# Performance work log

Hardware: AMD Instinct MI355X
Metric: run time of the kernel (lower is better)

The kernel has to match this reference:

```python
import jax, jax.numpy as jnp
import numpy as np

B, LQ, LK = 8, 1024, 1024
H, HD = 8, 128            # n_head, hidden_dim (per-head)
HEAD_DIM, CHILD_DIM = 512, 512
D_MODEL = HEAD_DIM + CHILD_DIM
TEMP = float(np.sqrt(HD))
NEG = 100000000.0
EPS = 1e-5


def setup_inputs() -> dict:
    key = jax.random.key(0)
    ks = jax.random.split(key, 12)
    q = jax.random.normal(ks[0], (B, LQ, HEAD_DIM), jnp.float32)
    k = jax.random.normal(ks[1], (B, LK, CHILD_DIM), jnp.float32)
    v = jax.random.normal(ks[2], (B, LK, D_MODEL), jnp.float32)
    old_score = 0.1 * jax.random.normal(ks[3], (H * B, LQ, LK), jnp.float32)
    float_mask = (jax.random.uniform(ks[4], (B, LQ, LK)) > 0.2).astype(jnp.float32)
    # torch nn.Linear weights are [out_features, in_features]
    wq = jax.random.normal(ks[5], (H * HD, HEAD_DIM), jnp.float32) * np.sqrt(2.0 / (HEAD_DIM + HD))
    wk = jax.random.normal(ks[6], (H * HD, CHILD_DIM), jnp.float32) * np.sqrt(2.0 / (CHILD_DIM + HD))
    wv = jax.random.normal(ks[7], (H * HD, D_MODEL), jnp.float32) * np.sqrt(2.0 / (D_MODEL + HD))
    wfc = jax.random.normal(ks[8], (D_MODEL, H * HD), jnp.float32) * np.sqrt(2.0 / (D_MODEL + H * HD))
    bq = jnp.zeros((H * HD,), jnp.float32)
    bk = jnp.zeros((H * HD,), jnp.float32)
    bv = jnp.zeros((H * HD,), jnp.float32)
    bfc = jnp.zeros((D_MODEL,), jnp.float32)
    ln_g = jnp.ones((D_MODEL,), jnp.float32)
    ln_b = jnp.zeros((D_MODEL,), jnp.float32)
    return dict(q=q, k=k, v=v, old_score=old_score, float_mask=float_mask,
                wq=wq, bq=bq, wk=wk, bk=bk, wv=wv, bv=bv,
                wfc=wfc, bfc=bfc, ln_g=ln_g, ln_b=ln_b)


def reference(q, k, v, old_score, float_mask, wq, bq, wk, bk, wv, bv, wfc, bfc, ln_g, ln_b):
    b, lq, _ = q.shape
    lk = k.shape[1]
    residual = v
    qh = (q @ wq.T + bq).reshape(b, lq, H, HD)   # [b,lq,h,d]
    kh = (k @ wk.T + bk).reshape(b, lk, H, HD)
    vh = (v @ wv.T + bv).reshape(b, lk, H, HD)
    # raw_score laid out head-major to match torch's (n_head*B, Lq, Lk)
    raw = jnp.einsum('bqhd,bkhd->hbqk', qh, kh) + old_score.reshape(H, b, lq, lk)
    score = raw - NEG * (1.0 - float_mask)[None]          # broadcast over heads
    attn = jax.nn.softmax(score / TEMP, axis=-1)          # eval path
    out = jnp.einsum('hbqk,bkhd->bqhd', attn, vh).reshape(b, lq, H * HD)
    out = out @ wfc.T + bfc + residual                    # dropout=identity (eval)
    mean = jnp.mean(out, axis=-1, keepdims=True)
    var = jnp.mean(jnp.square(out - mean), axis=-1, keepdims=True)
    out = (out - mean) / jnp.sqrt(var + EPS) * ln_g + ln_b
    return out, raw.reshape(H * b, lq, lk)
```

## Files before the change

kernel.cpp:

```cpp
#include <hip/hip_runtime.h>

typedef unsigned short u16;
typedef __bf16 bf16x8 __attribute__((ext_vector_type(8)));
typedef float f32x4 __attribute__((ext_vector_type(4)));

#define MFMA16(a,b,c) __builtin_amdgcn_mfma_f32_16x16x32_bf16(a,b,c,0,0,0)

static __device__ __forceinline__ u16 f2bf(float f){
  unsigned u = __builtin_bit_cast(unsigned, f);
  u += 0x7fffu + ((u>>16)&1u);
  return (u16)(u>>16);
}
static __device__ __forceinline__ int swz256(int r,int c){ return r*256 + (c ^ ((r&7)<<4)); }
static __device__ __forceinline__ int swz128(int r,int c){ return r*128 + (c ^ ((r&7)<<4)); }

__global__ void conv_f2b(const float* __restrict__ in, u16* __restrict__ out, int n4){
  int i = blockIdx.x*256 + threadIdx.x;
  if (i >= n4) return;
  float4 f = reinterpret_cast<const float4*>(in)[i];
  ushort4 o; o.x=f2bf(f.x); o.y=f2bf(f.y); o.z=f2bf(f.z); o.w=f2bf(f.w);
  reinterpret_cast<ushort4*>(out)[i] = o;
}

template<int MODE>
__global__ __launch_bounds__(256) void gemm_nt(const u16* __restrict__ A, const u16* __restrict__ Bw,
    const float* __restrict__ bias, const float* __restrict__ resid,
    u16* __restrict__ Cb, float* __restrict__ Cf, int M, int N, int K)
{
  __shared__ uint4 ldsv[2048];
  char* la = (char*)ldsv;
  char* lb = la + 16384;
  const int tid = threadIdx.x, lane = tid&63, w = tid>>6;
  const int l15 = lane&15, l4 = lane>>4;
  const int wm = w&1, wn = w>>1;
  const int mb = blockIdx.x, nb = blockIdx.y;
  const f32x4 zero4 = {0.f,0.f,0.f,0.f};
  f32x4 acc[4][4];
  #pragma unroll
  for (int i=0;i<4;++i)
    #pragma unroll
    for (int j=0;j<4;++j) acc[i][j] = zero4;

  for (int k0=0;k0<K;k0+=64){
    __syncthreads();
    #pragma unroll
    for (int it=0; it<4; ++it){
      int idx = tid + it*256;
      int row = idx>>3, c = idx&7;
      uint4 va = *reinterpret_cast<const uint4*>(A + (size_t)(mb*128+row)*K + k0 + c*8);
      *reinterpret_cast<uint4*>(la + swz128(row, c*16)) = va;
      uint4 vb = *reinterpret_cast<const uint4*>(Bw + (size_t)(nb*128+row)*K + k0 + c*8);
      *reinterpret_cast<uint4*>(lb + swz128(row, c*16)) = vb;
    }
    __syncthreads();
    #pragma unroll
    for (int kk=0;kk<2;++kk){
      bf16x8 af[4], bfr[4];
      #pragma unroll
      for (int i=0;i<4;++i){
        af[i]  = *reinterpret_cast<const bf16x8*>(la + swz128(wm*64+i*16+l15, (kk*32+l4*8)*2));
        bfr[i] = *reinterpret_cast<const bf16x8*>(lb + swz128(wn*64+i*16+l15, (kk*32+l4*8)*2));
      }
      #pragma unroll
      for (int i=0;i<4;++i)
        #pragma unroll
        for (int j=0;j<4;++j)
          acc[i][j] = MFMA16(af[i], bfr[j], acc[i][j]);
    }
  }
  #pragma unroll
  for (int j=0;j<4;++j){
    int col = nb*128 + wn*64 + j*16 + l15;
    float bv = bias[col];
    #pragma unroll
    for (int i=0;i<4;++i){
      int row0 = mb*128 + wm*64 + i*16 + l4*4;
      if (MODE == 0){
        #pragma unroll
        for (int r=0;r<4;++r)
          Cb[(size_t)(row0+r)*N + col] = f2bf(acc[i][j][r] + bv);
      } else if (MODE == 1){
        int bb = row0 >> 10, kp = row0 & 1023;
        ushort4 o;
        o.x = f2bf(acc[i][j][0]+bv); o.y = f2bf(acc[i][j][1]+bv);
        o.z = f2bf(acc[i][j][2]+bv); o.w = f2bf(acc[i][j][3]+bv);
        *reinterpret_cast<ushort4*>(Cb + (size_t)(bb*1024+col)*1024 + kp) = o;
      } else {
        #pragma unroll
        for (int r=0;r<4;++r){
          size_t off = (size_t)(row0+r)*N + col;
          Cf[off] = acc[i][j][r] + bv + resid[off];
        }
      }
    }
  }
}

__global__ __launch_bounds__(256) void attn_fused(const u16* __restrict__ qh,
    const u16* __restrict__ kh, const u16* __restrict__ vt,
    const float* __restrict__ oldsc, const float* __restrict__ fmask,
    float* __restrict__ raw, u16* __restrict__ ao)
{
  __shared__ uint4 ldsv[2560];
  char* lk_ = (char*)ldsv;
  char* lv_ = lk_ + 16384;
  char* lp_ = lk_ + 32768;
  const int tid = threadIdx.x, lane = tid&63, w = tid>>6;
  const int l15 = lane&15, l4 = lane>>4;
  const int qb = blockIdx.x, b = blockIdx.y, h = blockIdx.z;
  const float invT = 0.088388347648318447f;
  const f32x4 zero4 = {0.f,0.f,0.f,0.f};

  bf16x8 qf[4];
  {
    const u16* qp = qh + (size_t)(b*1024 + qb*64 + w*16 + l15)*1024 + h*128 + l4*8;
    #pragma unroll
    for (int kk=0;kk<4;++kk)
      qf[kk] = __builtin_bit_cast(bf16x8, *reinterpret_cast<const uint4*>(qp + kk*32));
  }
  f32x4 oacc[8];
  #pragma unroll
  for (int i=0;i<8;++i) oacc[i] = zero4;
  float mr[4], lr[4];
  #pragma unroll
  for (int r=0;r<4;++r){ mr[r] = -3.0e38f; lr[r] = 0.f; }

  for (int kt=0; kt<16; ++kt){
    __syncthreads();
    #pragma unroll
    for (int it=0; it<4; ++it){
      int idx = tid + it*256;
      { int row = idx>>4, c = idx&15;
        uint4 t = *reinterpret_cast<const uint4*>(kh + (size_t)(b*1024 + kt*64 + row)*1024 + h*128 + c*8);
        *reinterpret_cast<uint4*>(lk_ + swz256(row, c*16)) = t; }
      { int row = idx>>3, c = idx&7;
        uint4 t = *reinterpret_cast<const uint4*>(vt + (size_t)(b*1024 + h*128 + row)*1024 + kt*64 + c*8);
        *reinterpret_cast<uint4*>(lv_ + swz128(row, c*16)) = t; }
    }
    __syncthreads();
    f32x4 fs[4];
    #pragma unroll
    for (int fj=0;fj<4;++fj){
      f32x4 s = zero4;
      #pragma unroll
      for (int kk=0;kk<4;++kk){
        bf16x8 kf = *reinterpret_cast<const bf16x8*>(lk_ + swz256(fj*16+l15, (kk*32+l4*8)*2));
        s = MFMA16(qf[kk], kf, s);
      }
      fs[fj] = s;
    }
    const int qglob = qb*64 + w*16 + l4*4;
    size_t rbase  = ((size_t)(h*8 + b)*1024 + qglob)*1024 + kt*64;
    size_t mbase2 = ((size_t)b*1024 + qglob)*1024 + kt*64;
    float tm[4];
    #pragma unroll
    for (int r=0;r<4;++r){
      float mx = -3.0e38f;
      #pragma unroll
      for (int fj=0;fj<4;++fj){
        int kvc = fj*16 + l15;
        float old = oldsc[rbase + (size_t)r*1024 + kvc];
        float rv = fs[fj][r] + old;
        raw[rbase + (size_t)r*1024 + kvc] = rv;
        float mk = fmask[mbase2 + (size_t)r*1024 + kvc];
        float sc = (rv - 1.0e8f*(1.0f - mk)) * invT;
        fs[fj][r] = sc;
        mx = fmaxf(mx, sc);
      }
      tm[r] = mx;
    }
    #pragma unroll
    for (int o=1;o<16;o<<=1){
      #pragma unroll
      for (int r=0;r<4;++r) tm[r] = fmaxf(tm[r], __shfl_xor(tm[r], o));
    }
    #pragma unroll
    for (int r=0;r<4;++r){
      float mn  = fmaxf(mr[r], tm[r]);
      float esc = __expf(mr[r] - mn);
      mr[r] = mn;
      lr[r] *= esc;
      #pragma unroll
      for (int nf=0;nf<8;++nf) oacc[nf][r] *= esc;
      int prow = w*16 + l4*4 + r;
      #pragma unroll
      for (int fj=0;fj<4;++fj){
        float p = __expf(fs[fj][r] - mn);
        lr[r] += p;
        *reinterpret_cast<u16*>(lp_ + swz128(prow, (fj*16+l15)*2)) = f2bf(p);
      }
    }
    #pragma unroll
    for (int kkv=0;kkv<2;++kkv){
      bf16x8 pf = *reinterpret_cast<const bf16x8*>(lp_ + swz128(w*16+l15, (kkv*32+l4*8)*2));
      #pragma unroll
      for (int nf=0;nf<8;++nf){
        bf16x8 vf = *reinterpret_cast<const bf16x8*>(lv_ + swz128(nf*16+l15, (kkv*32+l4*8)*2));
        oacc[nf] = MFMA16(pf, vf, oacc[nf]);
      }
    }
  }
  #pragma unroll
  for (int o=1;o<16;o<<=1){
    #pragma unroll
    for (int r=0;r<4;++r) lr[r] += __shfl_xor(lr[r], o);
  }
  #pragma unroll
  for (int nf=0;nf<8;++nf){
    int col = h*128 + nf*16 + l15;
    #pragma unroll
    for (int r=0;r<4;++r){
      size_t orow = (size_t)(b*1024 + qb*64 + w*16 + l4*4 + r);
      ao[orow*1024 + col] = f2bf(oacc[nf][r] * (1.0f/lr[r]));
    }
  }
}

__global__ __launch_bounds__(256) void ln_k(float* __restrict__ io,
    const float* __restrict__ g, const float* __restrict__ bb)
{
  const int lane = threadIdx.x & 63, w = threadIdx.x >> 6;
  size_t row = (size_t)blockIdx.x*4 + w;
  float4* p = reinterpret_cast<float4*>(io + row*1024);
  float4 x[4];
  float s = 0.f, s2 = 0.f;
  #pragma unroll
  for (int i=0;i<4;++i){
    x[i] = p[lane + i*64];
    s  += x[i].x + x[i].y + x[i].z + x[i].w;
    s2 += x[i].x*x[i].x + x[i].y*x[i].y + x[i].z*x[i].z + x[i].w*x[i].w;
  }
  #pragma unroll
  for (int o=1;o<64;o<<=1){ s += __shfl_xor(s,o); s2 += __shfl_xor(s2,o); }
  float mean = s * 0.0009765625f;
  float var  = s2 * 0.0009765625f - mean*mean;
  float rstd = rsqrtf(var + 1e-5f);
  const float4* gp = reinterpret_cast<const float4*>(g);
  const float4* bp = reinterpret_cast<const float4*>(bb);
  #pragma unroll
  for (int i=0;i<4;++i){
    float4 gg = gp[lane+i*64], bv = bp[lane+i*64], y;
    y.x = (x[i].x-mean)*rstd*gg.x + bv.x;
    y.y = (x[i].y-mean)*rstd*gg.y + bv.y;
    y.z = (x[i].z-mean)*rstd*gg.z + bv.z;
    y.w = (x[i].w-mean)*rstd*gg.w + bv.w;
    p[lane+i*64] = y;
  }
}

extern "C" void kernel_launch(void* const* d_in, const int* in_sizes, int n_in,
                              void* d_out, int out_size, void* d_ws, size_t ws_size,
                              hipStream_t stream)
{
  const float* q    = (const float*)d_in[0];
  const float* k    = (const float*)d_in[1];
  const float* v    = (const float*)d_in[2];
  const float* olds = (const float*)d_in[3];
  const float* fm   = (const float*)d_in[4];
  const float* wq   = (const float*)d_in[5];
  const float* bq   = (const float*)d_in[6];
  const float* wk   = (const float*)d_in[7];
  const float* bk   = (const float*)d_in[8];
  const float* wv   = (const float*)d_in[9];
  const float* bv   = (const float*)d_in[10];
  const float* wfc  = (const float*)d_in[11];
  const float* bfc  = (const float*)d_in[12];
  const float* lng  = (const float*)d_in[13];
  const float* lnb  = (const float*)d_in[14];
  float* out = (float*)d_out;
  float* raw = out + 8388608;

  u16* ws  = (u16*)d_ws;
  u16* qbf = ws;
  u16* kbf = qbf + 4194304;
  u16* vbf = kbf + 4194304;
  u16* wqb = vbf + 8388608;
  u16* wkb = wqb + 524288;
  u16* wvb = wkb + 524288;
  u16* wfb = wvb + 1048576;
  u16* qhb = wfb + 1048576;
  u16* khb = qhb + 8388608;
  u16* vtb = khb + 8388608;
  u16* aob = vtb + 8388608;

  conv_f2b<<<4096,256,0,stream>>>(q,   qbf, 1048576);
  conv_f2b<<<4096,256,0,stream>>>(k,   kbf, 1048576);
  conv_f2b<<<8192,256,0,stream>>>(v,   vbf, 2097152);
  conv_f2b<<<512, 256,0,stream>>>(wq,  wqb, 131072);
  conv_f2b<<<512, 256,0,stream>>>(wk,  wkb, 131072);
  conv_f2b<<<1024,256,0,stream>>>(wv,  wvb, 262144);
  conv_f2b<<<1024,256,0,stream>>>(wfc, wfb, 262144);

  gemm_nt<0><<<dim3(64,8),256,0,stream>>>(qbf, wqb, bq, nullptr, qhb, nullptr, 8192,1024,512);
  gemm_nt<0><<<dim3(64,8),256,0,stream>>>(kbf, wkb, bk, nullptr, khb, nullptr, 8192,1024,512);
  gemm_nt<1><<<dim3(64,8),256,0,stream>>>(vbf, wvb, bv, nullptr, vtb, nullptr, 8192,1024,1024);

  attn_fused<<<dim3(16,8,8),256,0,stream>>>(qhb, khb, vtb, olds, fm, raw, aob);

  gemm_nt<2><<<dim3(64,8),256,0,stream>>>(aob, wfb, bfc, v, nullptr, out, 8192,1024,1024);
  ln_k<<<2048,256,0,stream>>>(out, lng, lnb);
}
```

Before: 319.2 us.

## Use direct global-to-LDS loads and vectorize score/mask/raw accesses in attention

Replaces register-staged global loads plus LDS stores with global_load_lds direct-to-LDS transfers in both the GEMM and attention kernels, pre-swizzling source columns so the MFMA read layout is preserved. In attention, K rows are permuted so each lane's four score columns are contiguous, which turns the old_score and mask reads and the raw store into float4 accesses and the P write into a single ushort4 store. The old_score and mask loads are also issued before the barrier so they overlap with the tile load. The approach depends on the row permutation and swizzle exactly matching what the MFMA fragment reads expect, so any mismatch would give wrong results.

```diff
diff --git a/kernel.cpp b/kernel.cpp
--- a/kernel.cpp
+++ b/kernel.cpp
@@ -13,6 +13,12 @@
 }
 static __device__ __forceinline__ int swz256(int r,int c){ return r*256 + (c ^ ((r&7)<<4)); }
 static __device__ __forceinline__ int swz128(int r,int c){ return r*128 + (c ^ ((r&7)<<4)); }
+
+static __device__ __forceinline__ void gload16(const void* g, void* l){
+  __builtin_amdgcn_global_load_lds(
+      (const __attribute__((address_space(1))) unsigned int*)g,
+      (__attribute__((address_space(3))) unsigned int*)l, 16, 0, 0);
+}
 
 __global__ void conv_f2b(const float* __restrict__ in, u16* __restrict__ out, int n4){
   int i = blockIdx.x*256 + threadIdx.x;
@@ -45,12 +51,10 @@
     __syncthreads();
     #pragma unroll
     for (int it=0; it<4; ++it){
-      int idx = tid + it*256;
-      int row = idx>>3, c = idx&7;
-      uint4 va = *reinterpret_cast<const uint4*>(A + (size_t)(mb*128+row)*K + k0 + c*8);
-      *reinterpret_cast<uint4*>(la + swz128(row, c*16)) = va;
-      uint4 vb = *reinterpret_cast<const uint4*>(Bw + (size_t)(nb*128+row)*K + k0 + c*8);
-      *reinterpret_cast<uint4*>(lb + swz128(row, c*16)) = vb;
+      int slot = it*256 + tid;
+      int r = slot>>3, cg = (slot&7) ^ (r&7);
+      gload16(A + (size_t)(mb*128+r)*K + k0 + cg*8, la + (it*256 + w*64)*16);
+      gload16(Bw + (size_t)(nb*128+r)*K + k0 + cg*8, lb + (it*256 + w*64)*16);
     }
     __syncthreads();
     #pragma unroll
@@ -125,17 +129,29 @@
   #pragma unroll
   for (int r=0;r<4;++r){ mr[r] = -3.0e38f; lr[r] = 0.f; }
 
+  const int qglob = qb*64 + w*16 + l4*4;
+
   for (int kt=0; kt<16; ++kt){
     __syncthreads();
     #pragma unroll
     for (int it=0; it<4; ++it){
-      int idx = tid + it*256;
-      { int row = idx>>4, c = idx&15;
-        uint4 t = *reinterpret_cast<const uint4*>(kh + (size_t)(b*1024 + kt*64 + row)*1024 + h*128 + c*8);
-        *reinterpret_cast<uint4*>(lk_ + swz256(row, c*16)) = t; }
-      { int row = idx>>3, c = idx&7;
-        uint4 t = *reinterpret_cast<const uint4*>(vt + (size_t)(b*1024 + h*128 + row)*1024 + kt*64 + c*8);
-        *reinterpret_cast<uint4*>(lv_ + swz128(row, c*16)) = t; }
+      int slot = it*256 + tid;
+      { int rs = slot>>4, cs = slot&15;
+        int cg = cs ^ (rs&7);
+        int kv = (rs&15)*4 + (rs>>4);
+        gload16(kh + (size_t)(b*1024 + kt*64 + kv)*1024 + h*128 + cg*8,
+                lk_ + (it*256 + w*64)*16); }
+      { int r = slot>>3, cg = (slot&7) ^ (r&7);
+        gload16(vt + (size_t)(b*1024 + h*128 + r)*1024 + kt*64 + cg*8,
+                lv_ + (it*256 + w*64)*16); }
+    }
+    size_t rbase = ((size_t)(h*8 + b)*1024 + qglob)*1024 + kt*64 + l15*4;
+    size_t mbase = ((size_t)b*1024 + qglob)*1024 + kt*64 + l15*4;
+    float4 o4[4], m4[4];
+    #pragma unroll
+    for (int r=0;r<4;++r){
+      o4[r] = *reinterpret_cast<const float4*>(oldsc + rbase + (size_t)r*1024);
+      m4[r] = *reinterpret_cast<const float4*>(fmask + mbase + (size_t)r*1024);
     }
     __syncthreads();
     f32x4 fs[4];
@@ -149,25 +165,18 @@
       }
       fs[fj] = s;
     }
-    const int qglob = qb*64 + w*16 + l4*4;
-    size_t rbase  = ((size_t)(h*8 + b)*1024 + qglob)*1024 + kt*64;
-    size_t mbase2 = ((size_t)b*1024 + qglob)*1024 + kt*64;
     float tm[4];
     #pragma unroll
     for (int r=0;r<4;++r){
-      float mx = -3.0e38f;
-      #pragma unroll
-      for (int fj=0;fj<4;++fj){
-        int kvc = fj*16 + l15;
-        float old = oldsc[rbase + (size_t)r*1024 + kvc];
-        float rv = fs[fj][r] + old;
-        raw[rbase + (size_t)r*1024 + kvc] = rv;
-        float mk = fmask[mbase2 + (size_t)r*1024 + kvc];
-        float sc = (rv - 1.0e8f*(1.0f - mk)) * invT;
-        fs[fj][r] = sc;
-        mx = fmaxf(mx, sc);
-      }
-      tm[r] = mx;
+      float4 rv;
+      rv.x = fs[0][r] + o4[r].x; rv.y = fs[1][r] + o4[r].y;
+      rv.z = fs[2][r] + o4[r].z; rv.w = fs[3][r] + o4[r].w;
+      *reinterpret_cast<float4*>(raw + rbase + (size_t)r*1024) = rv;
+      fs[0][r] = (rv.x - 1.0e8f*(1.0f - m4[r].x)) * invT;
+      fs[1][r] = (rv.y - 1.0e8f*(1.0f - m4[r].y)) * invT;
+      fs[2][r] = (rv.z - 1.0e8f*(1.0f - m4[r].z)) * invT;
+      fs[3][r] = (rv.w - 1.0e8f*(1.0f - m4[r].w)) * invT;
+      tm[r] = fmaxf(fmaxf(fs[0][r], fs[1][r]), fmaxf(fs[2][r], fs[3][r]));
     }
     #pragma unroll
     for (int o=1;o<16;o<<=1){
@@ -182,13 +191,13 @@
       lr[r] *= esc;
       #pragma unroll
       for (int nf=0;nf<8;++nf) oacc[nf][r] *= esc;
+      float px = __expf(fs[0][r] - mn), py = __expf(fs[1][r] - mn);
+      float pz = __expf(fs[2][r] - mn), pw = __expf(fs[3][r] - mn);
+      lr[r] += px + py + pz + pw;
+      ushort4 o;
+      o.x = f2bf(px); o.y = f2bf(py); o.z = f2bf(pz); o.w = f2bf(pw);
       int prow = w*16 + l4*4 + r;
-      #pragma unroll
-      for (int fj=0;fj<4;++fj){
-        float p = __expf(fs[fj][r] - mn);
-        lr[r] += p;
-        *reinterpret_cast<u16*>(lp_ + swz128(prow, (fj*16+l15)*2)) = f2bf(p);
-      }
+      *reinterpret_cast<ushort4*>(lp_ + swz128(prow, l15*8)) = o;
     }
     #pragma unroll
     for (int kkv=0;kkv<2;++kkv){
```

Measured after the change: 316.1 us. About the same (-1.0%).
